# Performance work log

Measured on AMD Instinct MI355X. Metric: run time of the kernel, lower is better.

## Reference

```python
import jax, jax.numpy as jnp
import numpy as np

B, T, S, H = 4, 128, 512, 512
LN_EPS = 1e-5


def setup_inputs() -> dict:
    key = jax.random.key(0)
    ks = jax.random.split(key, 10)
    query = jax.random.normal(ks[0], (B, T, H), dtype=jnp.float32)
    encoder_outputs = jax.random.normal(ks[1], (B, S, H), dtype=jnp.float32)
    src_lengths = jax.random.randint(ks[2], (B,), 1, S + 1, dtype=jnp.int32)
    # Parameters (nn.Linear stores weight as (out, in); we apply x @ W.T)
    W_h = jax.random.normal(ks[3], (H, H), dtype=jnp.float32) / np.sqrt(H)
    W_s = jax.random.normal(ks[4], (H, H), dtype=jnp.float32) / np.sqrt(H)
    v = jax.random.normal(ks[5], (H,), dtype=jnp.float32) * 0.01
    W_out = jax.random.normal(ks[6], (H, 2 * H), dtype=jnp.float32) / np.sqrt(2 * H)
    b_out = jnp.zeros((H,), dtype=jnp.float32)
    gamma = jnp.ones((H,), dtype=jnp.float32)
    beta = jnp.zeros((H,), dtype=jnp.float32)
    return {
        "query": query, "encoder_outputs": encoder_outputs, "src_lengths": src_lengths,
        "W_h": W_h, "W_s": W_s, "v": v, "W_out": W_out, "b_out": b_out,
        "gamma": gamma, "beta": beta,
    }


def reference(query, encoder_outputs, src_lengths, W_h, W_s, v, W_out, b_out, gamma, beta):
    # Project query and encoder states: (b,t,h) and (b,s,h)
    q_proj = jnp.einsum('bth,oh->bto', query, W_s)
    k_proj = jnp.einsum('bsh,oh->bso', encoder_outputs, W_h)
    # Additive score: tanh over broadcast-add, then dot with v -> (b,t,s)
    score = jnp.einsum('btsh,h->bts', jnp.tanh(q_proj[:, :, None, :] + k_proj[:, None, :, :]), v)
    # Mask padded source positions (src_idx >= length)
    pad = jnp.arange(S)[None, :] >= src_lengths[:, None]          # (b,s)
    score = jnp.where(pad[:, None, :], -jnp.inf, score)
    attn = jax.nn.softmax(score, axis=-1)                          # (b,t,s)
    context = jnp.einsum('bts,bsh->bth', attn, encoder_outputs)    # (b,t,h)
    cq = jnp.concatenate([context, query], axis=-1)                # (b,t,2h)
    out = jnp.tanh(jnp.einsum('btk,ok->bto', cq, W_out) + b_out)
    # LayerNorm over last dim
    mu = jnp.mean(out, axis=-1, keepdims=True)
    var = jnp.mean(jnp.square(out - mu), axis=-1, keepdims=True)
    return (out - mu) / jnp.sqrt(var + LN_EPS) * gamma + beta
```

## Files before the change

### kernel.cpp

```cpp
#include <hip/hip_runtime.h>
#include <hip/hip_bf16.h>
#include <math.h>

#define B 4
#define T 128
#define S 512
#define H 512
#define QK_SCALE 2.8853900817779268f

#if defined(__has_builtin)
#if __has_builtin(__builtin_amdgcn_exp2f)
#define EXP2F(x) __builtin_amdgcn_exp2f(x)
#else
#define EXP2F(x) __expf((x) * 0.6931471805599453f)
#endif
#else
#define EXP2F(x) __expf((x) * 0.6931471805599453f)
#endif

typedef __attribute__((ext_vector_type(8))) short bf16x8;
typedef __attribute__((ext_vector_type(4))) float f32x4;

__device__ __forceinline__ short f2b(float x) {
    unsigned int u = __float_as_uint(x);
    u += 0x7fffu + ((u >> 16) & 1u);
    return (short)(u >> 16);
}
__device__ __forceinline__ float fast_tanh(float x) {
    float e = __expf(2.0f * x);
    float r = __builtin_amdgcn_rcpf(e + 1.0f);
    return 1.0f - 2.0f * r;
}

__global__ __launch_bounds__(256) void cvt_all(
    const float* __restrict__ q, const float* __restrict__ Ws,
    const float* __restrict__ Wh, const float* __restrict__ Wo,
    const float* __restrict__ enc,
    short* __restrict__ qb, short* __restrict__ wsb, short* __restrict__ whb,
    short* __restrict__ wob, short* __restrict__ eb, short* __restrict__ encT) {
    const int bid = blockIdx.x;
    const int tid = threadIdx.x;
    if (bid >= 1152) {
        __shared__ short tb[32][33];
        const int bid2 = bid - 1152;
        const int b = bid2 >> 8, s0 = ((bid2 >> 4) & 15) * 32, h0 = (bid2 & 15) * 32;
        const int r = tid >> 3, c = (tid & 7) * 4;
        float4 a = *(const float4*)&enc[((size_t)(b * S + s0 + r)) * H + h0 + c];
        tb[c + 0][r] = f2b(a.x); tb[c + 1][r] = f2b(a.y);
        tb[c + 2][r] = f2b(a.z); tb[c + 3][r] = f2b(a.w);
        __syncthreads();
        ushort4 o = make_ushort4((unsigned short)tb[r][c], (unsigned short)tb[r][c + 1],
                                 (unsigned short)tb[r][c + 2], (unsigned short)tb[r][c + 3]);
        *(ushort4*)&encT[((size_t)(b * H + h0 + r)) * S + s0 + c] = o;
        return;
    }
    size_t i = ((size_t)bid * 256 + tid) * 8;
    const float* src; short* dst; size_t off;
    if (i < 262144)        { src = q;   dst = qb;  off = i; }
    else if (i < 524288)   { src = Ws;  dst = wsb; off = i - 262144; }
    else if (i < 786432)   { src = Wh;  dst = whb; off = i - 524288; }
    else if (i < 1310720)  { src = Wo;  dst = wob; off = i - 786432; }
    else                   { src = enc; dst = eb;  off = i - 1310720; }
    float4 a = *(const float4*)(src + off);
    float4 b = *(const float4*)(src + off + 4);
    ushort4 o0 = make_ushort4((unsigned short)f2b(a.x), (unsigned short)f2b(a.y),
                              (unsigned short)f2b(a.z), (unsigned short)f2b(a.w));
    ushort4 o1 = make_ushort4((unsigned short)f2b(b.x), (unsigned short)f2b(b.y),
                              (unsigned short)f2b(b.z), (unsigned short)f2b(b.w));
    *(ushort4*)(dst + off) = o0;
    *(ushort4*)(dst + off + 4) = o1;
}

#define MFMA4(APTR0, APTR1, BPTR0, BPTR1, KOFF)                                  \
    {                                                                            \
        bf16x8 a0 = *(const bf16x8*)((APTR0) + (KOFF));                          \
        bf16x8 a1 = *(const bf16x8*)((APTR1) + (KOFF));                          \
        bf16x8 b0 = *(const bf16x8*)((BPTR0) + (KOFF));                          \
        bf16x8 b1 = *(const bf16x8*)((BPTR1) + (KOFF));                          \
        acc00 = __builtin_amdgcn_mfma_f32_16x16x32_bf16(a0, b0, acc00, 0, 0, 0); \
        acc01 = __builtin_amdgcn_mfma_f32_16x16x32_bf16(a0, b1, acc01, 0, 0, 0); \
        acc10 = __builtin_amdgcn_mfma_f32_16x16x32_bf16(a1, b0, acc10, 0, 0, 0); \
        acc11 = __builtin_amdgcn_mfma_f32_16x16x32_bf16(a1, b1, acc11, 0, 0, 0); \
    }

__global__ __launch_bounds__(64) void mfma_proj(
    const short* __restrict__ qb, const short* __restrict__ eb,
    const short* __restrict__ wsb, const short* __restrict__ whb,
    float* __restrict__ qe, float* __restrict__ ke) {
    const int lane = threadIdx.x;
    const int r = lane & 15, kb = lane >> 4;
    const int n0 = blockIdx.x * 32;
    const int m0 = blockIdx.y * 32;
    const short* A; const short* W; float* C;
    if (m0 < 512) { A = qb + (size_t)m0 * H; W = wsb; C = qe + (size_t)m0 * H; }
    else { A = eb + (size_t)(m0 - 512) * H; W = whb; C = ke + (size_t)(m0 - 512) * H; }
    const short* a0p = A + (size_t)r * H + kb * 8;
    const short* a1p = a0p + 16 * H;
    const short* b0p = W + (size_t)(n0 + r) * H + kb * 8;
    const short* b1p = b0p + 16 * H;
    f32x4 acc00 = {0,0,0,0}, acc01 = {0,0,0,0}, acc10 = {0,0,0,0}, acc11 = {0,0,0,0};
#pragma unroll 4
    for (int k = 0; k < H; k += 32) MFMA4(a0p, a1p, b0p, b1p, k)
    const int cr = kb * 4, cc = r;
#pragma unroll
    for (int g = 0; g < 4; ++g) {
        C[(size_t)(cr + g) * H + n0 + cc]           = EXP2F(acc00[g] * QK_SCALE);
        C[(size_t)(cr + g) * H + n0 + 16 + cc]      = EXP2F(acc01[g] * QK_SCALE);
        C[(size_t)(16 + cr + g) * H + n0 + cc]      = EXP2F(acc10[g] * QK_SCALE);
        C[(size_t)(16 + cr + g) * H + n0 + 16 + cc] = EXP2F(acc11[g] * QK_SCALE);
    }
}

__global__ __launch_bounds__(64) void score_v3(
    const float* __restrict__ qe, const float* __restrict__ ke,
    const float* __restrict__ v, const int* __restrict__ slen,
    float* __restrict__ scoreh) {
    const int qt = blockIdx.z & 3;
    const int b = blockIdx.z >> 2;
    const int L = slen[b];
    const int sbase = blockIdx.x * 8;
    if (sbase >= L) return;
    const int tbase = blockIdx.y * 8;
    const int hbase = qt * 128;
    __shared__ __align__(16) float qs[8][132];
    __shared__ __align__(16) float ks[8][132];
    __shared__ __align__(16) float vsh[128];
    const int lane = threadIdx.x;
    {
        const int r = lane >> 3, c = (lane & 7) * 16;
        const float* qsrc = qe + (size_t)(b * T + tbase + r) * H + hbase + c;
        const float* ksrc = ke + (size_t)(b * S + sbase + r) * H + hbase + c;
#pragma unroll
        for (int j = 0; j < 4; ++j) {
            *(float4*)&qs[r][c + j * 4] = *(const float4*)(qsrc + j * 4);
            *(float4*)&ks[r][c + j * 4] = *(const float4*)(ksrc + j * 4);
        }
        float2 vv = *(const float2*)&v[hbase + lane * 2];
        *(float2*)&vsh[lane * 2] = make_float2(-2.f * vv.x, -2.f * vv.y);
    }
    __syncthreads();
    const int t = lane >> 3, s = lane & 7;
    const float* qrow = &qs[t][0];
    const float* krow = &ks[s][0];
    float a0 = 0.f, a1 = 0.f, a2 = 0.f, a3 = 0.f;
#pragma unroll 4
    for (int i = 0; i < 128; i += 4) {
        float4 q4 = *(const float4*)&qrow[i];
        float4 k4 = *(const float4*)&krow[i];
        float4 v4 = *(const float4*)&vsh[i];
        a0 = fmaf(v4.x, __builtin_amdgcn_rcpf(fmaf(q4.x, k4.x, 1.f)), a0);
        a1 = fmaf(v4.y, __builtin_amdgcn_rcpf(fmaf(q4.y, k4.y, 1.f)), a1);
        a2 = fmaf(v4.z, __builtin_amdgcn_rcpf(fmaf(q4.z, k4.z, 1.f)), a2);
        a3 = fmaf(v4.w, __builtin_amdgcn_rcpf(fmaf(q4.w, k4.w, 1.f)), a3);
    }
    scoreh[((size_t)qt * (B * T) + b * T + tbase + t) * S + sbase + s] =
        (a0 + a1) + (a2 + a3);
}

__global__ __launch_bounds__(256) void softmax_k(
    const float* __restrict__ scoreh, const int* __restrict__ slen,
    short* __restrict__ attnb) {
    __shared__ float red[8];
    const int row = blockIdx.x;
    const int L = slen[row >> 7];
    const int tid = threadIdx.x;
    const int lane = tid & 63, wv = tid >> 6;
    const size_t sl = (size_t)(B * T) * S;
    const float* p0 = scoreh + (size_t)row * S;
    float x0 = p0[tid] + p0[sl + tid] + p0[2 * sl + tid] + p0[3 * sl + tid];
    float x1 = p0[tid + 256] + p0[sl + tid + 256] + p0[2 * sl + tid + 256] +
               p0[3 * sl + tid + 256];
    if (tid >= L) x0 = -INFINITY;
    if (tid + 256 >= L) x1 = -INFINITY;
    float m = fmaxf(x0, x1);
#pragma unroll
    for (int off = 32; off > 0; off >>= 1) m = fmaxf(m, __shfl_xor(m, off));
    if (lane == 0) red[wv] = m;
    __syncthreads();
    m = fmaxf(fmaxf(red[0], red[1]), fmaxf(red[2], red[3]));
    float e0 = __expf(x0 - m);
    float e1 = __expf(x1 - m);
    float sm = e0 + e1;
#pragma unroll
    for (int off = 32; off > 0; off >>= 1) sm += __shfl_xor(sm, off);
    if (lane == 0) red[4 + wv] = sm;
    __syncthreads();
    float inv = 1.0f / (red[4] + red[5] + red[6] + red[7]);
    short* o = attnb + (size_t)row * S;
    o[tid] = f2b(e0 * inv);
    o[tid + 256] = f2b(e1 * inv);
}

__global__ __launch_bounds__(64) void mfma_ctx(
    const short* __restrict__ attnb, const short* __restrict__ encT,
    const int* __restrict__ slen, short* __restrict__ ctxb) {
    const int b = blockIdx.z;
    const int L = slen[b];
    const int Keff = min(S, (L + 31) & ~31);
    const int lane = threadIdx.x;
    const int r = lane & 15, kb = lane >> 4;
    const int m0 = blockIdx.y * 32;
    const int n0 = blockIdx.x * 32;
    const short* A = attnb + (size_t)(b * T + m0) * S;
    const short* Bp = encT + (size_t)b * H * S;
    const short* a0p = A + (size_t)r * S + kb * 8;
    const short* a1p = a0p + 16 * S;
    const short* b0p = Bp + (size_t)(n0 + r) * S + kb * 8;
    const short* b1p = b0p + 16 * S;
    f32x4 acc00 = {0,0,0,0}, acc01 = {0,0,0,0}, acc10 = {0,0,0,0}, acc11 = {0,0,0,0};
#pragma unroll 2
    for (int k = 0; k < Keff; k += 32) MFMA4(a0p, a1p, b0p, b1p, k)
    const int cr = kb * 4, cc = r;
#pragma unroll
    for (int g = 0; g < 4; ++g) {
        size_t row0 = (size_t)(b * T + m0 + cr + g) * H;
        size_t row1 = (size_t)(b * T + m0 + 16 + cr + g) * H;
        ctxb[row0 + n0 + cc]      = f2b(acc00[g]);
        ctxb[row0 + n0 + 16 + cc] = f2b(acc01[g]);
        ctxb[row1 + n0 + cc]      = f2b(acc10[g]);
        ctxb[row1 + n0 + 16 + cc] = f2b(acc11[g]);
    }
}

__global__ __launch_bounds__(64) void mfma_out(
    const short* __restrict__ ctxb, const short* __restrict__ qb,
    const short* __restrict__ wob, const float* __restrict__ bias,
    float* __restrict__ pre) {
    const int lane = threadIdx.x;
    const int r = lane & 15, kb = lane >> 4;
    const int m0 = blockIdx.y * 32, n0 = blockIdx.x * 32;
    f32x4 acc00 = {0,0,0,0}, acc01 = {0,0,0,0}, acc10 = {0,0,0,0}, acc11 = {0,0,0,0};
    const short* b0p = wob + (size_t)(n0 + r) * (2 * H) + kb * 8;
    const short* b1p = b0p + 16 * (2 * H);
    {
        const short* a0p = ctxb + (size_t)(m0 + r) * H + kb * 8;
        const short* a1p = a0p + 16 * H;
#pragma unroll 4
        for (int k = 0; k < H; k += 32) MFMA4(a0p, a1p, b0p, b1p, k)
    }
    {
        const short* a0p = qb + (size_t)(m0 + r) * H + kb * 8;
        const short* a1p = a0p + 16 * H;
        const short* c0p = b0p + H;
        const short* c1p = b1p + H;
#pragma unroll 4
        for (int k = 0; k < H; k += 32) MFMA4(a0p, a1p, c0p, c1p, k)
    }
    const int cr = kb * 4, cc = r;
    float bn0 = bias[n0 + cc], bn1 = bias[n0 + 16 + cc];
#pragma unroll
    for (int g = 0; g < 4; ++g) {
        size_t row0 = (size_t)(m0 + cr + g) * H;
        size_t row1 = (size_t)(m0 + 16 + cr + g) * H;
        pre[row0 + n0 + cc]      = fast_tanh(acc00[g] + bn0);
        pre[row0 + n0 + 16 + cc] = fast_tanh(acc01[g] + bn1);
        pre[row1 + n0 + cc]      = fast_tanh(acc10[g] + bn0);
        pre[row1 + n0 + 16 + cc] = fast_tanh(acc11[g] + bn1);
    }
}

__global__ __launch_bounds__(256) void ln_out(
    const float* __restrict__ X, const float* __restrict__ gamma,
    const float* __restrict__ beta, float* __restrict__ out) {
    __shared__ float red[8];
    const int r = blockIdx.x;
    const int tid = threadIdx.x;
    const int lane = tid & 63, wv = tid >> 6;
    const float* x = X + (size_t)r * H;
    float x0 = x[tid], x1 = x[tid + 256];
    float s = x0 + x1;
#pragma unroll
    for (int off = 32; off > 0; off >>= 1) s += __shfl_down(s, off);
    if (lane == 0) red[wv] = s;
    __syncthreads();
    float mu = (red[0] + red[1] + red[2] + red[3]) * (1.0f / H);
    float d0 = x0 - mu, d1 = x1 - mu;
    float vsum = d0 * d0 + d1 * d1;
#pragma unroll
    for (int off = 32; off > 0; off >>= 1) vsum += __shfl_down(vsum, off);
    if (lane == 0) red[4 + wv] = vsum;
    __syncthreads();
    float var = (red[4] + red[5] + red[6] + red[7]) * (1.0f / H);
    float inv = rsqrtf(var + 1e-5f);
    out[(size_t)r * H + tid] = d0 * inv * gamma[tid] + beta[tid];
    out[(size_t)r * H + tid + 256] = d1 * inv * gamma[tid + 256] + beta[tid + 256];
}

extern "C" void kernel_launch(void* const* d_in, const int* in_sizes, int n_in,
                              void* d_out, int out_size, void* d_ws, size_t ws_size,
                              hipStream_t stream) {
    const float* query = (const float*)d_in[0];
    const float* enc   = (const float*)d_in[1];
    const int*   slen  = (const int*)d_in[2];
    const float* W_h   = (const float*)d_in[3];
    const float* W_s   = (const float*)d_in[4];
    const float* v     = (const float*)d_in[5];
    const float* W_out = (const float*)d_in[6];
    const float* b_out = (const float*)d_in[7];
    const float* gamma = (const float*)d_in[8];
    const float* beta  = (const float*)d_in[9];
    float* out = (float*)d_out;

    char* base = (char*)d_ws;
    short* qb     = (short*)(base + 0);
    short* wsb    = (short*)(base + 524288);
    short* whb    = (short*)(base + 1048576);
    short* wob    = (short*)(base + 1572864);
    short* eb     = (short*)(base + 2621440);
    float* qe     = (float*)(base + 4718592);
    float* ke     = (float*)(base + 5767168);
    float* scoreh = (float*)(base + 9961472);
    short* attnb  = (short*)(base + 14155776);
    short* encT   = (short*)(base + 14680064);
    short* ctxb   = (short*)(base + 16777216);
    float* pre    = (float*)(base + 17301504);

    cvt_all<<<dim3(2176), dim3(256), 0, stream>>>(query, W_s, W_h, W_out, enc,
                                                  qb, wsb, whb, wob, eb, encT);
    mfma_proj<<<dim3(16, 80), dim3(64), 0, stream>>>(qb, eb, wsb, whb, qe, ke);
    score_v3<<<dim3(64, 16, 16), dim3(64), 0, stream>>>(qe, ke, v, slen, scoreh);
    softmax_k<<<dim3(B * T), dim3(256), 0, stream>>>(scoreh, slen, attnb);
    mfma_ctx<<<dim3(16, 4, 4), dim3(64), 0, stream>>>(attnb, encT, slen, ctxb);
    mfma_out<<<dim3(16, 16), dim3(64), 0, stream>>>(ctxb, qb, wob, b_out, pre);
    ln_out<<<dim3(B * T), dim3(256), 0, stream>>>(pre, gamma, beta, out);
}
```

Baseline: 66.75 us.

## Fuse bf16 conversion into GEMM loads, merge softmax with transpose, widen score tiles

Drops the separate fp32-to-bf16 conversion kernel. The projection and output GEMMs now load fp32 inputs and convert in registers, and the encoder transpose moves into a combined softmax/transpose kernel. The projection also skips key rows beyond each source length. The score kernel computes two source positions per lane (16 per block) so each query load is reused. This removes one launch and a full round trip of bf16 copies, at the cost of reading fp32 operands twice as wide and repeating the conversions across GEMM tiles.

```diff
diff --git a/kernel.cpp b/kernel.cpp
--- a/kernel.cpp
+++ b/kernel.cpp
@@ -31,18 +31,123 @@
     float r = __builtin_amdgcn_rcpf(e + 1.0f);
     return 1.0f - 2.0f * r;
 }
-
-__global__ __launch_bounds__(256) void cvt_all(
-    const float* __restrict__ q, const float* __restrict__ Ws,
-    const float* __restrict__ Wh, const float* __restrict__ Wo,
-    const float* __restrict__ enc,
-    short* __restrict__ qb, short* __restrict__ wsb, short* __restrict__ whb,
-    short* __restrict__ wob, short* __restrict__ eb, short* __restrict__ encT) {
+__device__ __forceinline__ bf16x8 ld_cvt8(const float* p) {
+    float4 a = *(const float4*)p;
+    float4 c = *(const float4*)(p + 4);
+    bf16x8 r;
+    r[0] = f2b(a.x); r[1] = f2b(a.y); r[2] = f2b(a.z); r[3] = f2b(a.w);
+    r[4] = f2b(c.x); r[5] = f2b(c.y); r[6] = f2b(c.z); r[7] = f2b(c.w);
+    return r;
+}
+
+#define MFMA_STEP(A0, A1, B0, B1)                                                \
+    {                                                                            \
+        acc00 = __builtin_amdgcn_mfma_f32_16x16x32_bf16(A0, B0, acc00, 0, 0, 0); \
+        acc01 = __builtin_amdgcn_mfma_f32_16x16x32_bf16(A0, B1, acc01, 0, 0, 0); \
+        acc10 = __builtin_amdgcn_mfma_f32_16x16x32_bf16(A1, B0, acc10, 0, 0, 0); \
+        acc11 = __builtin_amdgcn_mfma_f32_16x16x32_bf16(A1, B1, acc11, 0, 0, 0); \
+    }
+
+__global__ __launch_bounds__(64) void mfma_proj(
+    const float* __restrict__ query, const float* __restrict__ enc,
+    const float* __restrict__ Ws, const float* __restrict__ Wh,
+    const int* __restrict__ slen, float* __restrict__ qe, float* __restrict__ ke) {
+    const int lane = threadIdx.x;
+    const int r = lane & 15, kb = lane >> 4;
+    const int n0 = blockIdx.x * 32;
+    const int m0 = blockIdx.y * 32;
+    const float* A; const float* W; float* C;
+    if (m0 < 512) { A = query + (size_t)m0 * H; W = Ws; C = qe + (size_t)m0 * H; }
+    else {
+        const int row = m0 - 512;
+        if ((row & 511) >= slen[row >> 9]) return;
+        A = enc + (size_t)row * H; W = Wh; C = ke + (size_t)row * H;
+    }
+    const float* a0p = A + (size_t)r * H + kb * 8;
+    const float* a1p = a0p + 16 * H;
+    const float* b0p = W + (size_t)(n0 + r) * H + kb * 8;
+    const float* b1p = b0p + 16 * H;
+    f32x4 acc00 = {0,0,0,0}, acc01 = {0,0,0,0}, acc10 = {0,0,0,0}, acc11 = {0,0,0,0};
+#pragma unroll 4
+    for (int k = 0; k < H; k += 32) {
+        bf16x8 a0 = ld_cvt8(a0p + k), a1 = ld_cvt8(a1p + k);
+        bf16x8 b0 = ld_cvt8(b0p + k), b1 = ld_cvt8(b1p + k);
+        MFMA_STEP(a0, a1, b0, b1)
+    }
+    const int cr = kb * 4, cc = r;
+#pragma unroll
+    for (int g = 0; g < 4; ++g) {
+        C[(size_t)(cr + g) * H + n0 + cc]           = EXP2F(acc00[g] * QK_SCALE);
+        C[(size_t)(cr + g) * H + n0 + 16 + cc]      = EXP2F(acc01[g] * QK_SCALE);
+        C[(size_t)(16 + cr + g) * H + n0 + cc]      = EXP2F(acc10[g] * QK_SCALE);
+        C[(size_t)(16 + cr + g) * H + n0 + 16 + cc] = EXP2F(acc11[g] * QK_SCALE);
+    }
+}
+
+__global__ __launch_bounds__(64) void score_v4(
+    const float* __restrict__ qe, const float* __restrict__ ke,
+    const float* __restrict__ v, const int* __restrict__ slen,
+    float* __restrict__ scoreh) {
+    const int qt = blockIdx.z & 3;
+    const int b = blockIdx.z >> 2;
+    const int L = slen[b];
+    const int sbase = blockIdx.x * 16;
+    if (sbase >= L) return;
+    const int tbase = blockIdx.y * 8;
+    const int hbase = qt * 128;
+    __shared__ __align__(16) float qs[8][132];
+    __shared__ __align__(16) float ks[16][132];
+    __shared__ __align__(16) float vsh[128];
+    const int lane = threadIdx.x;
+    {
+        const int r = lane >> 3, c = (lane & 7) * 16;
+        const float* qsrc = qe + (size_t)(b * T + tbase + r) * H + hbase + c;
+        const float* k0src = ke + (size_t)(b * S + sbase + r) * H + hbase + c;
+        const float* k1src = k0src + 8 * H;
+#pragma unroll
+        for (int j = 0; j < 4; ++j) {
+            *(float4*)&qs[r][c + j * 4] = *(const float4*)(qsrc + j * 4);
+            *(float4*)&ks[r][c + j * 4] = *(const float4*)(k0src + j * 4);
+            *(float4*)&ks[8 + r][c + j * 4] = *(const float4*)(k1src + j * 4);
+        }
+        float2 vv = *(const float2*)&v[hbase + lane * 2];
+        *(float2*)&vsh[lane * 2] = make_float2(-2.f * vv.x, -2.f * vv.y);
+    }
+    __syncthreads();
+    const int t = lane >> 3, s0 = (lane & 7) * 2;
+    const float* qrow = &qs[t][0];
+    const float* k0r = &ks[s0][0];
+    const float* k1r = &ks[s0 + 1][0];
+    float a0 = 0.f, a1 = 0.f, c0 = 0.f, c1 = 0.f;
+#pragma unroll 2
+    for (int i = 0; i < 128; i += 4) {
+        float4 q4 = *(const float4*)&qrow[i];
+        float4 ka = *(const float4*)&k0r[i];
+        float4 kb = *(const float4*)&k1r[i];
+        float4 v4 = *(const float4*)&vsh[i];
+        a0 = fmaf(v4.x, __builtin_amdgcn_rcpf(fmaf(q4.x, ka.x, 1.f)), a0);
+        c0 = fmaf(v4.x, __builtin_amdgcn_rcpf(fmaf(q4.x, kb.x, 1.f)), c0);
+        a1 = fmaf(v4.y, __builtin_amdgcn_rcpf(fmaf(q4.y, ka.y, 1.f)), a1);
+        c1 = fmaf(v4.y, __builtin_amdgcn_rcpf(fmaf(q4.y, kb.y, 1.f)), c1);
+        a0 = fmaf(v4.z, __builtin_amdgcn_rcpf(fmaf(q4.z, ka.z, 1.f)), a0);
+        c0 = fmaf(v4.z, __builtin_amdgcn_rcpf(fmaf(q4.z, kb.z, 1.f)), c0);
+        a1 = fmaf(v4.w, __builtin_amdgcn_rcpf(fmaf(q4.w, ka.w, 1.f)), a1);
+        c1 = fmaf(v4.w, __builtin_amdgcn_rcpf(fmaf(q4.w, kb.w, 1.f)), c1);
+    }
+    *(float2*)&scoreh[((size_t)qt * (B * T) + b * T + tbase + t) * S + sbase + s0] =
+        make_float2(a0 + a1, c0 + c1);
+}
+
+__global__ __launch_bounds__(256) void mid_kernel(
+    const float* __restrict__ scoreh, const int* __restrict__ slen,
+    short* __restrict__ attnb, const float* __restrict__ enc,
+    short* __restrict__ encT) {
+    __shared__ short tb[32][33];
+    __shared__ float red[8];
     const int bid = blockIdx.x;
     const int tid = threadIdx.x;
-    if (bid >= 1152) {
-        __shared__ short tb[32][33];
-        const int bid2 = bid - 1152;
+    if (bid >= 512) {
+        const int bid2 = bid - 512;
         const int b = bid2 >> 8, s0 = ((bid2 >> 4) & 15) * 32, h0 = (bid2 & 15) * 32;
         const int r = tid >> 3, c = (tid & 7) * 4;
         float4 a = *(const float4*)&enc[((size_t)(b * S + s0 + r)) * H + h0 + c];
@@ -54,116 +159,8 @@
         *(ushort4*)&encT[((size_t)(b * H + h0 + r)) * S + s0 + c] = o;
         return;
     }
-    size_t i = ((size_t)bid * 256 + tid) * 8;
-    const float* src; short* dst; size_t off;
-    if (i < 262144)        { src = q;   dst = qb;  off = i; }
-    else if (i < 524288)   { src = Ws;  dst = wsb; off = i - 262144; }
-    else if (i < 786432)   { src = Wh;  dst = whb; off = i - 524288; }
-    else if (i < 1310720)  { src = Wo;  dst = wob; off = i - 786432; }
-    else                   { src = enc; dst = eb;  off = i - 1310720; }
-    float4 a = *(const float4*)(src + off);
-    float4 b = *(const float4*)(src + off + 4);
-    ushort4 o0 = make_ushort4((unsigned short)f2b(a.x), (unsigned short)f2b(a.y),
-                              (unsigned short)f2b(a.z), (unsigned short)f2b(a.w));
-    ushort4 o1 = make_ushort4((unsigned short)f2b(b.x), (unsigned short)f2b(b.y),
-                              (unsigned short)f2b(b.z), (unsigned short)f2b(b.w));
-    *(ushort4*)(dst + off) = o0;
-    *(ushort4*)(dst + off + 4) = o1;
-}
-
-#define MFMA4(APTR0, APTR1, BPTR0, BPTR1, KOFF)                                  \
-    {                                                                            \
-        bf16x8 a0 = *(const bf16x8*)((APTR0) + (KOFF));                          \
-        bf16x8 a1 = *(const bf16x8*)((APTR1) + (KOFF));                          \
-        bf16x8 b0 = *(const bf16x8*)((BPTR0) + (KOFF));                          \
-        bf16x8 b1 = *(const bf16x8*)((BPTR1) + (KOFF));                          \
-        acc00 = __builtin_amdgcn_mfma_f32_16x16x32_bf16(a0, b0, acc00, 0, 0, 0); \
-        acc01 = __builtin_amdgcn_mfma_f32_16x16x32_bf16(a0, b1, acc01, 0, 0, 0); \
-        acc10 = __builtin_amdgcn_mfma_f32_16x16x32_bf16(a1, b0, acc10, 0, 0, 0); \
-        acc11 = __builtin_amdgcn_mfma_f32_16x16x32_bf16(a1, b1, acc11, 0, 0, 0); \
-    }
-
-__global__ __launch_bounds__(64) void mfma_proj(
-    const short* __restrict__ qb, const short* __restrict__ eb,
-    const short* __restrict__ wsb, const short* __restrict__ whb,
-    float* __restrict__ qe, float* __restrict__ ke) {
-    const int lane = threadIdx.x;
-    const int r = lane & 15, kb = lane >> 4;
-    const int n0 = blockIdx.x * 32;
-    const int m0 = blockIdx.y * 32;
-    const short* A; const short* W; float* C;
-    if (m0 < 512) { A = qb + (size_t)m0 * H; W = wsb; C = qe + (size_t)m0 * H; }
-    else { A = eb + (size_t)(m0 - 512) * H; W = whb; C = ke + (size_t)(m0 - 512) * H; }
-    const short* a0p = A + (size_t)r * H + kb * 8;
-    const short* a1p = a0p + 16 * H;
-    const short* b0p = W + (size_t)(n0 + r) * H + kb * 8;
-    const short* b1p = b0p + 16 * H;
-    f32x4 acc00 = {0,0,0,0}, acc01 = {0,0,0,0}, acc10 = {0,0,0,0}, acc11 = {0,0,0,0};
-#pragma unroll 4
-    for (int k = 0; k < H; k += 32) MFMA4(a0p, a1p, b0p, b1p, k)
-    const int cr = kb * 4, cc = r;
-#pragma unroll
-    for (int g = 0; g < 4; ++g) {
-        C[(size_t)(cr + g) * H + n0 + cc]           = EXP2F(acc00[g] * QK_SCALE);
-        C[(size_t)(cr + g) * H + n0 + 16 + cc]      = EXP2F(acc01[g] * QK_SCALE);
-        C[(size_t)(16 + cr + g) * H + n0 + cc]      = EXP2F(acc10[g] * QK_SCALE);
-        C[(size_t)(16 + cr + g) * H + n0 + 16 + cc] = EXP2F(acc11[g] * QK_SCALE);
-    }
-}
-
-__global__ __launch_bounds__(64) void score_v3(
-    const float* __restrict__ qe, const float* __restrict__ ke,
-    const float* __restrict__ v, const int* __restrict__ slen,
-    float* __restrict__ scoreh) {
-    const int qt = blockIdx.z & 3;
-    const int b = blockIdx.z >> 2;
-    const int L = slen[b];
-    const int sbase = blockIdx.x * 8;
-    if (sbase >= L) return;
-    const int tbase = blockIdx.y * 8;
-    const int hbase = qt * 128;
-    __shared__ __align__(16) float qs[8][132];
-    __shared__ __align__(16) float ks[8][132];
-    __shared__ __align__(16) float vsh[128];
-    const int lane = threadIdx.x;
-    {
-        const int r = lane >> 3, c = (lane & 7) * 16;
-        const float* qsrc = qe + (size_t)(b * T + tbase + r) * H + hbase + c;
-        const float* ksrc = ke + (size_t)(b * S + sbase + r) * H + hbase + c;
-#pragma unroll
-        for (int j = 0; j < 4; ++j) {
-            *(float4*)&qs[r][c + j * 4] = *(const float4*)(qsrc + j * 4);
-            *(float4*)&ks[r][c + j * 4] = *(const float4*)(ksrc + j * 4);
-        }
-        float2 vv = *(const float2*)&v[hbase + lane * 2];
-        *(float2*)&vsh[lane * 2] = make_float2(-2.f * vv.x, -2.f * vv.y);
-    }
-    __syncthreads();
-    const int t = lane >> 3, s = lane & 7;
-    const float* qrow = &qs[t][0];
-    const float* krow = &ks[s][0];
-    float a0 = 0.f, a1 = 0.f, a2 = 0.f, a3 = 0.f;
-#pragma unroll 4
-    for (int i = 0; i < 128; i += 4) {
-        float4 q4 = *(const float4*)&qrow[i];
-        float4 k4 = *(const float4*)&krow[i];
-        float4 v4 = *(const float4*)&vsh[i];
-        a0 = fmaf(v4.x, __builtin_amdgcn_rcpf(fmaf(q4.x, k4.x, 1.f)), a0);
-        a1 = fmaf(v4.y, __builtin_amdgcn_rcpf(fmaf(q4.y, k4.y, 1.f)), a1);
-        a2 = fmaf(v4.z, __builtin_amdgcn_rcpf(fmaf(q4.z, k4.z, 1.f)), a2);
-        a3 = fmaf(v4.w, __builtin_amdgcn_rcpf(fmaf(q4.w, k4.w, 1.f)), a3);
-    }
-    scoreh[((size_t)qt * (B * T) + b * T + tbase + t) * S + sbase + s] =
-        (a0 + a1) + (a2 + a3);
-}
-
-__global__ __launch_bounds__(256) void softmax_k(
-    const float* __restrict__ scoreh, const int* __restrict__ slen,
-    short* __restrict__ attnb) {
-    __shared__ float red[8];
-    const int row = blockIdx.x;
+    const int row = bid;
     const int L = slen[row >> 7];
-    const int tid = threadIdx.x;
     const int lane = tid & 63, wv = tid >> 6;
     const size_t sl = (size_t)(B * T) * S;
     const float* p0 = scoreh + (size_t)row * S;
@@ -209,7 +206,11 @@
     const short* b1p = b0p + 16 * S;
     f32x4 acc00 = {0,0,0,0}, acc01 = {0,0,0,0}, acc10 = {0,0,0,0}, acc11 = {0,0,0,0};
 #pragma unroll 2
-    for (int k = 0; k < Keff; k += 32) MFMA4(a0p, a1p, b0p, b1p, k)
+    for (int k = 0; k < Keff; k += 32) {
+        bf16x8 a0 = *(const bf16x8*)(a0p + k), a1 = *(const bf16x8*)(a1p + k);
+        bf16x8 b0 = *(const bf16x8*)(b0p + k), b1 = *(const bf16x8*)(b1p + k);
+        MFMA_STEP(a0, a1, b0, b1)
+    }
     const int cr = kb * 4, cc = r;
 #pragma unroll
     for (int g = 0; g < 4; ++g) {
@@ -223,28 +224,36 @@
 }
 
 __global__ __launch_bounds__(64) void mfma_out(
-    const short* __restrict__ ctxb, const short* __restrict__ qb,
-    const short* __restrict__ wob, const float* __restrict__ bias,
+    const short* __restrict__ ctxb, const float* __restrict__ query,
+    const float* __restrict__ Wo, const float* __restrict__ bias,
     float* __restrict__ pre) {
     const int lane = threadIdx.x;
     const int r = lane & 15, kb = lane >> 4;
     const int m0 = blockIdx.y * 32, n0 = blockIdx.x * 32;
     f32x4 acc00 = {0,0,0,0}, acc01 = {0,0,0,0}, acc10 = {0,0,0,0}, acc11 = {0,0,0,0};
-    const short* b0p = wob + (size_t)(n0 + r) * (2 * H) + kb * 8;
-    const short* b1p = b0p + 16 * (2 * H);
+    const float* b0p = Wo + (size_t)(n0 + r) * (2 * H) + kb * 8;
+    const float* b1p = b0p + 16 * (2 * H);
     {
         const short* a0p = ctxb + (size_t)(m0 + r) * H + kb * 8;
         const short* a1p = a0p + 16 * H;
 #pragma unroll 4
-        for (int k = 0; k < H; k += 32) MFMA4(a0p, a1p, b0p, b1p, k)
+        for (int k = 0; k < H; k += 32) {
+            bf16x8 a0 = *(const bf16x8*)(a0p + k), a1 = *(const bf16x8*)(a1p + k);
+            bf16x8 b0 = ld_cvt8(b0p + k), b1 = ld_cvt8(b1p + k);
+            MFMA_STEP(a0, a1, b0, b1)
+        }
     }
     {
-        const short* a0p = qb + (size_t)(m0 + r) * H + kb * 8;
-        const short* a1p = a0p + 16 * H;
-        const short* c0p = b0p + H;
-        const short* c1p = b1p + H;
+        const float* a0p = query + (size_t)(m0 + r) * H + kb * 8;
+        const float* a1p = a0p + 16 * H;
+        const float* c0p = b0p + H;
+        const float* c1p = b1p + H;
 #pragma unroll 4
-        for (int k = 0; k < H; k += 32) MFMA4(a0p, a1p, c0p, c1p, k)
+        for (int k = 0; k < H; k += 32) {
+            bf16x8 a0 = ld_cvt8(a0p + k), a1 = ld_cvt8(a1p + k);
+            bf16x8 b0 = ld_cvt8(c0p + k), b1 = ld_cvt8(c1p + k);
+            MFMA_STEP(a0, a1, b0, b1)
+        }
     }
     const int cr = kb * 4, cc = r;
     float bn0 = bias[n0 + cc], bn1 = bias[n0 + 16 + cc];
@@ -302,25 +311,18 @@
     float* out = (float*)d_out;
 
     char* base = (char*)d_ws;
-    short* qb     = (short*)(base + 0);
-    short* wsb    = (short*)(base + 524288);
-    short* whb    = (short*)(base + 1048576);
-    short* wob    = (short*)(base + 1572864);
-    short* eb     = (short*)(base + 2621440);
-    float* qe     = (float*)(base + 4718592);
-    float* ke     = (float*)(base + 5767168);
-    float* scoreh = (float*)(base + 9961472);
-    short* attnb  = (short*)(base + 14155776);
-    short* encT   = (short*)(base + 14680064);
-    short* ctxb   = (short*)(base + 16777216);
-    float* pre    = (float*)(base + 17301504);
-
-    cvt_all<<<dim3(2176), dim3(256), 0, stream>>>(query, W_s, W_h, W_out, enc,
-                                                  qb, wsb, whb, wob, eb, encT);
-    mfma_proj<<<dim3(16, 80), dim3(64), 0, stream>>>(qb, eb, wsb, whb, qe, ke);
-    score_v3<<<dim3(64, 16, 16), dim3(64), 0, stream>>>(qe, ke, v, slen, scoreh);
-    softmax_k<<<dim3(B * T), dim3(256), 0, stream>>>(scoreh, slen, attnb);
+    float* qe     = (float*)(base + 0);
+    float* ke     = (float*)(base + 1048576);
+    float* scoreh = (float*)(base + 5242880);
+    short* attnb  = (short*)(base + 9437184);
+    short* encT   = (short*)(base + 9961472);
+    short* ctxb   = (short*)(base + 12058624);
+    float* pre    = (float*)(base + 12582912);
+
+    mfma_proj<<<dim3(16, 80), dim3(64), 0, stream>>>(query, enc, W_s, W_h, slen, qe, ke);
+    score_v4<<<dim3(32, 16, 16), dim3(64), 0, stream>>>(qe, ke, v, slen, scoreh);
+    mid_kernel<<<dim3(1536), dim3(256), 0, stream>>>(scoreh, slen, attnb, enc, encT);
     mfma_ctx<<<dim3(16, 4, 4), dim3(64), 0, stream>>>(attnb, encT, slen, ctxb);
-    mfma_out<<<dim3(16, 16), dim3(64), 0, stream>>>(ctxb, qb, wob, b_out, pre);
+    mfma_out<<<dim3(16, 16), dim3(64), 0, stream>>>(ctxb, query, W_out, b_out, pre);
     ln_out<<<dim3(B * T), dim3(256), 0, stream>>>(pre, gamma, beta, out);
 }
```

After: 91.72 us. +37.4%, slower.
